# Optimization experiments

Hardware: AMD Instinct MI355X
Metric: run time of the kernel (lower is better)

Reference implementation:

```python
import jax, jax.numpy as jnp
import numpy as np

D_MODEL, D_K, D_V = 1024, 128, 128
B, S = 8, 2048


def setup_inputs() -> dict:
    key = jax.random.key(0)
    k1, k2, k3, k4, k5 = jax.random.split(key, 5)
    x = jax.random.normal(k1, (B, S, D_MODEL), dtype=jnp.float32)
    enc_embed = jax.random.normal(k2, (B, S, D_MODEL), dtype=jnp.float32)
    # xavier_normal-ish init: std = sqrt(2/(fan_in+fan_out))
    W_Q = jax.random.normal(k3, (D_MODEL, D_K), dtype=jnp.float32) * np.sqrt(2.0 / (D_MODEL + D_K))
    W_K = jax.random.normal(k4, (D_MODEL, D_K), dtype=jnp.float32) * np.sqrt(2.0 / (D_MODEL + D_K))
    W_V = jax.random.normal(k5, (D_MODEL, D_V), dtype=jnp.float32) * np.sqrt(2.0 / (D_MODEL + D_V))
    return {"x": x, "enc_embed": enc_embed, "W_Q": W_Q, "W_K": W_K, "W_V": W_V}


def reference(x, enc_embed, W_Q, W_K, W_V):
    # use_enc_embed=False, use_mask=False path (self-attention)
    q = jnp.einsum('bsd,dk->bsk', x, W_Q)  # [B,S,d_k]
    k = jnp.einsum('bsd,dk->bsk', x, W_K)  # [B,S,d_k]
    v = jnp.einsum('bsd,dv->bsv', x, W_V)  # [B,S,d_v]
    scale = 1.0 / jnp.sqrt(jnp.asarray(D_K, dtype=x.dtype))
    scores = jnp.einsum('bqk,bsk->bqs', q, k) * scale  # [B,S,S]
    weights = jax.nn.softmax(scores, axis=-1)
    return jnp.einsum('bqs,bsv->bqv', weights, v)  # [B,S,d_v]
```

## Files before the change

### kernel.cpp

```cpp
#include <hip/hip_runtime.h>
#include <hip/hip_bf16.h>
#include <stdint.h>

typedef __attribute__((ext_vector_type(8))) short bf16x8;
typedef __attribute__((ext_vector_type(4))) float f32x4;
typedef __attribute__((ext_vector_type(4))) unsigned short u16x4;
typedef unsigned short u16;

#define D_MODEL 1024
#define DK 128
#define BATCH 8
#define SEQ 2048
#define NROWS (BATCH * SEQ)
#define NSPLIT 4
#define KVPB 512
#define NIT 16

static __device__ __forceinline__ void gl_lds16(const void* g, void* l) {
  __builtin_amdgcn_global_load_lds((const __attribute__((address_space(1))) void*)g,
                                   (__attribute__((address_space(3))) void*)l, 16, 0, 0);
}

static __device__ __forceinline__ u16 f2b(float f) {
  __hip_bfloat16 h = __float2bfloat16(f);
  return *reinterpret_cast<u16*>(&h);
}

static __device__ __forceinline__ uint32_t cvtpk(float lo, float hi) {
  uint32_t r;
  asm("v_cvt_pk_bf16_f32 %0, %1, %2" : "=v"(r) : "v"(lo), "v"(hi));
  return r;
}

static __device__ __forceinline__ float exp2hw(float x) {
  float r;
  asm("v_exp_f32 %0, %1" : "=v"(r) : "v"(x));
  return r;
}

__global__ __launch_bounds__(256) void wcvt(const float* __restrict__ wq,
                                            const float* __restrict__ wk,
                                            const float* __restrict__ wv,
                                            u16* __restrict__ wt3) {
  const int idx = blockIdx.x * 256 + threadIdx.x;
  int w = idx >> 17, rr = idx & 131071, k = rr >> 7, n = rr & 127;
  const float* W = (w == 0) ? wq : ((w == 1) ? wk : wv);
  int np = w * 128 + n;
  int kt = k >> 6;
  int slot = ((k >> 3) & 7) ^ ((np >> 1) & 7);
  size_t dst = ((size_t)kt * 3072 + np * 8 + slot) * 8 + (k & 7);
  wt3[dst] = f2b(W[k * DK + n]);
}

__global__ __launch_bounds__(512, 1) void qkv_gemm(const float* __restrict__ x,
                                                   const u16* __restrict__ wt3,
                                                   u16* __restrict__ qb,
                                                   u16* __restrict__ kb,
                                                   u16* __restrict__ vt) {
  __shared__ char sm[131072] __attribute__((aligned(16)));
  const int tid = threadIdx.x;
  const int lane = tid & 63;
  const int w = tid >> 6;
  const int g = lane >> 4;
  const int l15 = lane & 15;
  const int mt = blockIdx.x;
  const int wm = w >> 2, wn = w & 3;

  const char* aB = (const char*)x + (size_t)mt * 64 * 4096;
  const char* bB = (const char*)wt3;

  f32x4 acc[2][6];
#pragma unroll
  for (int i = 0; i < 2; ++i)
#pragma unroll
    for (int jj = 0; jj < 6; ++jj) acc[i][jj] = (f32x4){0.f, 0.f, 0.f, 0.f};

  auto stage = [&](int buf, int kt) {
    char* sA = sm + buf * 65536;
    char* sB = sA + 16384;
#pragma unroll
    for (int c = 0; c < 2; ++c) {
      int si = c * 512 + tid;
      int row = si >> 4;
      int s = si & 15;
      int gq = (s & 8) | ((s & 7) ^ (row & 7));
      gl_lds16(aB + (size_t)row * 4096 + kt * 256 + (gq << 4), sA + c * 8192 + w * 1024);
    }
    const char* bSrc = bB + (size_t)kt * 49152;
#pragma unroll
    for (int c = 0; c < 6; ++c) {
      gl_lds16(bSrc + (c * 512 + tid) * 16, sB + c * 8192 + w * 1024);
    }
  };

  auto compute = [&](const char* base) {
    const char* sA = base;
    const char* sB = base + 16384;
#pragma unroll
    for (int kk = 0; kk < 2; ++kk) {
      bf16x8 af[2];
#pragma unroll
      for (int mi = 0; mi < 2; ++mi) {
        int row = wm * 32 + mi * 16 + l15;
        f32x4 lo = *(const f32x4*)(sA + row * 256 +
                                   (((kk * 8) | ((2 * g + 0) ^ (row & 7))) << 4));
        f32x4 hi = *(const f32x4*)(sA + row * 256 +
                                   (((kk * 8) | ((2 * g + 1) ^ (row & 7))) << 4));
        union { uint32_t u[4]; bf16x8 v; } tt;
        tt.u[0] = cvtpk(lo[0], lo[1]);
        tt.u[1] = cvtpk(lo[2], lo[3]);
        tt.u[2] = cvtpk(hi[0], hi[1]);
        tt.u[3] = cvtpk(hi[2], hi[3]);
        af[mi] = tt.v;
      }
      bf16x8 bfr[6];
#pragma unroll
      for (int ni = 0; ni < 6; ++ni) {
        int np = wn * 96 + ni * 16 + l15;
        bfr[ni] = *(const bf16x8*)(sB + np * 128 +
                                   (((kk * 4 + g) ^ ((np >> 1) & 7)) << 4));
      }
      __builtin_amdgcn_s_setprio(1);
#pragma unroll
      for (int mi = 0; mi < 2; ++mi)
#pragma unroll
        for (int ni = 0; ni < 6; ++ni)
          acc[mi][ni] = __builtin_amdgcn_mfma_f32_16x16x32_bf16(af[mi], bfr[ni], acc[mi][ni], 0, 0, 0);
      __builtin_amdgcn_s_setprio(0);
    }
  };

  stage(0, 0);
#pragma unroll 1
  for (int t = 0; t < 16; ++t) {
    if (t < 15) {
      stage((t + 1) & 1, t + 1);
      asm volatile("s_waitcnt vmcnt(8)" ::: "memory");
    } else {
      asm volatile("s_waitcnt vmcnt(0)" ::: "memory");
    }
    __builtin_amdgcn_s_barrier();
    asm volatile("" ::: "memory");
    compute(sm + (t & 1) * 65536);
    asm volatile("" ::: "memory");
    __builtin_amdgcn_s_barrier();
  }

  const float qscale = 0.12751743f;
#pragma unroll
  for (int mi = 0; mi < 2; ++mi) {
#pragma unroll
    for (int ni = 0; ni < 6; ++ni) {
      int mbase = mt * 64 + wm * 32 + mi * 16 + g * 4;
      int np = wn * 96 + ni * 16 + l15;
      int ntd = np >> 7, n = np & 127;
      if (ntd == 2) {
        int b = mbase >> 11, s = mbase & 2047;
        int a = (s >> 2) & 7;
        int sp2 = (s & ~31) | ((((a & 3) << 1) | (a >> 2)) << 2);
        union { u16 u[4]; u16x4 v; } pk;
#pragma unroll
        for (int r2 = 0; r2 < 4; ++r2) pk.u[r2] = f2b(acc[mi][ni][r2]);
        *(u16x4*)((char*)vt + ((size_t)(b * 128 + n) * 2048 + sp2) * 2) = pk.v;
      } else {
        u16* dst = (ntd == 0) ? qb : kb;
        float sc = (ntd == 0) ? qscale : 1.0f;
#pragma unroll
        for (int r2 = 0; r2 < 4; ++r2)
          dst[(size_t)(mbase + r2) * 128 + n] = f2b(acc[mi][ni][r2] * sc);
      }
    }
  }
}

__global__ __launch_bounds__(256) void attn(const u16* __restrict__ qb,
                                            const u16* __restrict__ kb,
                                            const u16* __restrict__ vtg,
                                            u16* __restrict__ po,
                                            float* __restrict__ ls) {
  __shared__ char sm[49152] __attribute__((aligned(16)));
  const int tid = threadIdx.x, lane = tid & 63, w = tid >> 6;
  const int g = lane >> 4, l15 = lane & 15;
  const int id = blockIdx.x;
  const int wgid = ((id & 7) << 6) | (id >> 3);
  const int b = wgid >> 6, sp = (wgid >> 4) & 3, j = wgid & 15;
  const int s0q = j * 128 + w * 32;
  const int kv0 = sp * KVPB;

  const char* qB = (const char*)qb + (size_t)b * SEQ * 256;
  const char* kB = (const char*)kb + (size_t)b * SEQ * 256;
  const char* vB = (const char*)vtg + (size_t)b * 128 * SEQ * 2;

  bf16x8 qf[2][4];
#pragma unroll
  for (int h = 0; h < 2; ++h)
#pragma unroll
    for (int kk = 0; kk < 4; ++kk)
      qf[h][kk] = *(const bf16x8*)(qB + (size_t)(s0q + h * 16 + l15) * 256 + kk * 64 + g * 16);

  f32x4 o[2][8];
#pragma unroll
  for (int h = 0; h < 2; ++h)
#pragma unroll
    for (int i = 0; i < 8; ++i) o[h][i] = (f32x4){0.f, 0.f, 0.f, 0.f};
  float lsum[2] = {0.f, 0.f};

  char* sKb = sm;
  char* sVb = sm + 24576;

  auto stage = [&](int bi, int it) {
    char* sK = sKb + bi * 8192;
    char* sV = sVb + bi * 8192;
    int s0 = kv0 + it * 32;
#pragma unroll
    for (int c = 0; c < 2; ++c) {
      int base = c * 4096 + w * 1024;
      int L = base + lane * 16;
      {
        int row = L >> 8, col = L & 255;
        gl_lds16(kB + (size_t)(s0 + row) * 256 + (col ^ ((row & 7) << 4)), sK + base);
      }
      {
        int rv = L >> 6, cv = L & 63;
        gl_lds16(vB + (size_t)rv * 4096 + (size_t)s0 * 2 + (cv ^ ((rv & 3) << 4)), sV + base);
      }
    }
  };

  stage(0, 0);
  stage(1, 1);
  int cb = 0;
  for (int t = 0; t < NIT; ++t) {
    if (t < NIT - 1) asm volatile("s_waitcnt vmcnt(4)" ::: "memory");
    else asm volatile("s_waitcnt vmcnt(0)" ::: "memory");
    __builtin_amdgcn_s_barrier();
    if (t + 2 < NIT) {
      int sb = cb + 2;
      if (sb >= 3) sb -= 3;
      stage(sb, t + 2);
    }
    const char* sK = sKb + cb * 8192;
    const char* sV = sVb + cb * 8192;

    f32x4 st[2][2];
    st[0][0] = (f32x4){0.f, 0.f, 0.f, 0.f}; st[0][1] = st[0][0];
    st[1][0] = st[0][0]; st[1][1] = st[0][0];
    __builtin_amdgcn_s_setprio(1);
#pragma unroll
    for (int sub = 0; sub < 2; ++sub)
#pragma unroll
      for (int kk = 0; kk < 4; ++kk) {
        bf16x8 kf = *(const bf16x8*)(sK + (sub * 16 + l15) * 256 +
                                     ((kk * 64 + g * 16) ^ ((l15 & 7) << 4)));
        st[0][sub] = __builtin_amdgcn_mfma_f32_16x16x32_bf16(kf, qf[0][kk], st[0][sub], 0, 0, 0);
        st[1][sub] = __builtin_amdgcn_mfma_f32_16x16x32_bf16(kf, qf[1][kk], st[1][sub], 0, 0, 0);
      }
    __builtin_amdgcn_s_setprio(0);

    union U { uint32_t u[4]; bf16x8 v; } pf[2];
#pragma unroll
    for (int h = 0; h < 2; ++h) {
      float p[8];
#pragma unroll
      for (int sub = 0; sub < 2; ++sub)
#pragma unroll
        for (int r2 = 0; r2 < 4; ++r2) {
          float e = exp2hw(st[h][sub][r2]);
          lsum[h] += e;
          p[sub * 4 + r2] = e;
        }
      pf[h].u[0] = cvtpk(p[0], p[1]);
      pf[h].u[1] = cvtpk(p[2], p[3]);
      pf[h].u[2] = cvtpk(p[4], p[5]);
      pf[h].u[3] = cvtpk(p[6], p[7]);
    }

    __builtin_amdgcn_s_setprio(1);
#pragma unroll
    for (int dsub = 0; dsub < 8; ++dsub) {
      bf16x8 vf = *(const bf16x8*)(sV + (dsub * 16 + l15) * 64 +
                                   ((g * 16) ^ ((l15 & 3) << 4)));
      o[0][dsub] = __builtin_amdgcn_mfma_f32_16x16x32_bf16(vf, pf[0].v, o[0][dsub], 0, 0, 0);
      o[1][dsub] = __builtin_amdgcn_mfma_f32_16x16x32_bf16(vf, pf[1].v, o[1][dsub], 0, 0, 0);
    }
    __builtin_amdgcn_s_setprio(0);
    cb = (cb == 2) ? 0 : cb + 1;
  }

#pragma unroll
  for (int h = 0; h < 2; ++h) {
    lsum[h] += __shfl_xor(lsum[h], 16);
    lsum[h] += __shfl_xor(lsum[h], 32);
    int ridx = (b * 16 + j) * 128 + w * 32 + h * 16 + l15;
    u16* dst = po + ((size_t)sp * NROWS + ridx) * 128;
#pragma unroll
    for (int dsub = 0; dsub < 8; ++dsub) {
      union { uint32_t u[2]; u16x4 v; } pk2;
      pk2.u[0] = cvtpk(o[h][dsub][0], o[h][dsub][1]);
      pk2.u[1] = cvtpk(o[h][dsub][2], o[h][dsub][3]);
      *(u16x4*)(dst + dsub * 16 + g * 4) = pk2.v;
    }
    if (g == 0) ls[(size_t)sp * NROWS + ridx] = lsum[h];
  }
}

__global__ __launch_bounds__(256) void attn_combine(const u16* __restrict__ po,
                                                    const float* __restrict__ ls,
                                                    float* __restrict__ out) {
  int idx = blockIdx.x * 256 + threadIdx.x;
  int r = idx >> 4, d0 = (idx & 15) * 8;
  float denom = 0.f;
  float acc[8];
#pragma unroll
  for (int j = 0; j < 8; ++j) acc[j] = 0.f;
#pragma unroll
  for (int s = 0; s < NSPLIT; ++s) {
    denom += ls[(size_t)s * NROWS + r];
    bf16x8 v = *(const bf16x8*)(po + ((size_t)s * NROWS + r) * 128 + d0);
#pragma unroll
    for (int j = 0; j < 8; ++j) {
      uint32_t bits = ((uint32_t)(u16)v[j]) << 16;
      acc[j] += *reinterpret_cast<float*>(&bits);
    }
  }
  float inv = 1.0f / denom;
  f32x4 o0 = (f32x4){acc[0], acc[1], acc[2], acc[3]};
  f32x4 o1 = (f32x4){acc[4], acc[5], acc[6], acc[7]};
  *(f32x4*)(out + (size_t)r * 128 + d0) = o0 * inv;
  *(f32x4*)(out + (size_t)r * 128 + d0 + 4) = o1 * inv;
}

extern "C" void kernel_launch(void* const* d_in, const int* in_sizes, int n_in,
                              void* d_out, int out_size, void* d_ws, size_t ws_size,
                              hipStream_t stream) {
  const float* x = (const float*)d_in[0];
  const float* wq = (const float*)d_in[2];
  const float* wk = (const float*)d_in[3];
  const float* wv = (const float*)d_in[4];

  char* ws = (char*)d_ws;
  u16* po = (u16*)ws;
  float* ls = (float*)(ws + 16777216);
  u16* wt3 = (u16*)(ws + 17039360);
  u16* qb = (u16*)(ws + 17825792);
  u16* kb = (u16*)(ws + 22020096);
  u16* vt = (u16*)(ws + 26214400);
  float* out = (float*)d_out;

  wcvt<<<dim3(1536), dim3(256), 0, stream>>>(wq, wk, wv, wt3);
  qkv_gemm<<<dim3(256), dim3(512), 0, stream>>>(x, wt3, qb, kb, vt);
  attn<<<dim3(512), dim3(256), 0, stream>>>(qb, kb, vt, po, ls);
  attn_combine<<<dim3(1024), dim3(256), 0, stream>>>(po, ls, out);
}
```

Measured before the change: 63.78 us.

## Load QKV GEMM operands directly from global memory instead of LDS staging

Removes the double-buffered LDS staging (global_load_lds plus barriers) in the QKV projection GEMM and has each wave read its A (fp32 x) and B (bf16 weights) fragments straight from global memory into registers. This drops the 128KB LDS footprint, the block-level barriers and the explicit vmcnt pipeline. In exchange there is no cross-wave reuse through LDS, so the four column-waves reread the same A rows and weights through cache, and load latency is no longer hidden by explicit prefetch.

```diff
diff --git a/kernel.cpp b/kernel.cpp
--- a/kernel.cpp
+++ b/kernel.cpp
@@ -57,7 +57,6 @@
                                                    u16* __restrict__ qb,
                                                    u16* __restrict__ kb,
                                                    u16* __restrict__ vt) {
-  __shared__ char sm[131072] __attribute__((aligned(16)));
   const int tid = threadIdx.x;
   const int lane = tid & 63;
   const int w = tid >> 6;
@@ -75,37 +74,19 @@
 #pragma unroll
     for (int jj = 0; jj < 6; ++jj) acc[i][jj] = (f32x4){0.f, 0.f, 0.f, 0.f};
 
-  auto stage = [&](int buf, int kt) {
-    char* sA = sm + buf * 65536;
-    char* sB = sA + 16384;
-#pragma unroll
-    for (int c = 0; c < 2; ++c) {
-      int si = c * 512 + tid;
-      int row = si >> 4;
-      int s = si & 15;
-      int gq = (s & 8) | ((s & 7) ^ (row & 7));
-      gl_lds16(aB + (size_t)row * 4096 + kt * 256 + (gq << 4), sA + c * 8192 + w * 1024);
-    }
-    const char* bSrc = bB + (size_t)kt * 49152;
-#pragma unroll
-    for (int c = 0; c < 6; ++c) {
-      gl_lds16(bSrc + (c * 512 + tid) * 16, sB + c * 8192 + w * 1024);
-    }
-  };
-
-  auto compute = [&](const char* base) {
-    const char* sA = base;
-    const char* sB = base + 16384;
+  const char* aRow0 = aB + (size_t)(wm * 32 + 0 * 16 + l15) * 4096;
+  const char* aRow1 = aB + (size_t)(wm * 32 + 1 * 16 + l15) * 4096;
+
+#pragma unroll 2
+  for (int kt = 0; kt < 16; ++kt) {
 #pragma unroll
     for (int kk = 0; kk < 2; ++kk) {
       bf16x8 af[2];
 #pragma unroll
       for (int mi = 0; mi < 2; ++mi) {
-        int row = wm * 32 + mi * 16 + l15;
-        f32x4 lo = *(const f32x4*)(sA + row * 256 +
-                                   (((kk * 8) | ((2 * g + 0) ^ (row & 7))) << 4));
-        f32x4 hi = *(const f32x4*)(sA + row * 256 +
-                                   (((kk * 8) | ((2 * g + 1) ^ (row & 7))) << 4));
+        const char* ap = (mi ? aRow1 : aRow0) + kt * 256 + kk * 128 + g * 32;
+        f32x4 lo = *(const f32x4*)ap;
+        f32x4 hi = *(const f32x4*)(ap + 16);
         union { uint32_t u[4]; bf16x8 v; } tt;
         tt.u[0] = cvtpk(lo[0], lo[1]);
         tt.u[1] = cvtpk(lo[2], lo[3]);
@@ -117,8 +98,8 @@
 #pragma unroll
       for (int ni = 0; ni < 6; ++ni) {
         int np = wn * 96 + ni * 16 + l15;
-        bfr[ni] = *(const bf16x8*)(sB + np * 128 +
-                                   (((kk * 4 + g) ^ ((np >> 1) & 7)) << 4));
+        int slot = (kk * 4 + g) ^ ((np >> 1) & 7);
+        bfr[ni] = *(const bf16x8*)(bB + (size_t)kt * 49152 + np * 128 + slot * 16);
       }
       __builtin_amdgcn_s_setprio(1);
 #pragma unroll
@@ -128,22 +109,6 @@
           acc[mi][ni] = __builtin_amdgcn_mfma_f32_16x16x32_bf16(af[mi], bfr[ni], acc[mi][ni], 0, 0, 0);
       __builtin_amdgcn_s_setprio(0);
     }
-  };
-
-  stage(0, 0);
-#pragma unroll 1
-  for (int t = 0; t < 16; ++t) {
-    if (t < 15) {
-      stage((t + 1) & 1, t + 1);
-      asm volatile("s_waitcnt vmcnt(8)" ::: "memory");
-    } else {
-      asm volatile("s_waitcnt vmcnt(0)" ::: "memory");
-    }
-    __builtin_amdgcn_s_barrier();
-    asm volatile("" ::: "memory");
-    compute(sm + (t & 1) * 65536);
-    asm volatile("" ::: "memory");
-    __builtin_amdgcn_s_barrier();
   }
 
   const float qscale = 0.12751743f;
```

Result: slower. 96.05 us (+50.6%).
